# Performance work log

Hardware: AMD Instinct MI355X
Metric: run time of the kernel (lower is better)

## Reference

```python
import jax, jax.numpy as jnp
import numpy as np

DIM = 1024
N_HEADS = 16
HEAD_DIM = DIM // N_HEADS  # 64
B = 2
S = 2048
EPS = 1e-6  # flax LayerNorm default


def _layernorm(x, scale, bias):
    # LayerNorm over last axis with learnable scale and bias (flax defaults)
    mu = jnp.mean(x, axis=-1, keepdims=True)
    var = jnp.var(x, axis=-1, keepdims=True)
    return (x - mu) * jax.lax.rsqrt(var + EPS) * scale + bias


def _apply_rotary(t, sin, cos):
    # t: [b, s, h, hd]; sin/cos: [s, hd/2]
    tr = t.reshape(t.shape[:-1] + (-1, 2))
    r, i = tr[..., 0], tr[..., 1]            # [b, s, h, hd/2]
    c = cos[None, :, None, :]
    s_ = sin[None, :, None, :]
    out_r = r * c - i * s_
    out_i = r * s_ + i * c
    return jnp.stack([out_r, out_i], axis=-1).reshape(t.shape)


def setup_inputs() -> dict:
    key = jax.random.key(0)
    ks = jax.random.split(key, 8)
    x = jax.random.normal(ks[0], (B, S, DIM), dtype=jnp.float32)
    w_std = 1.0 / np.sqrt(DIM)  # ~lecun_normal scale
    wq = jax.random.normal(ks[1], (DIM, DIM), dtype=jnp.float32) * w_std
    wk = jax.random.normal(ks[2], (DIM, DIM), dtype=jnp.float32) * w_std
    wv = jax.random.normal(ks[3], (DIM, DIM), dtype=jnp.float32) * w_std
    wo = jax.random.normal(ks[4], (DIM, DIM), dtype=jnp.float32) * w_std
    # standard RoPE frequency table
    inv_freq = 1.0 / (10000.0 ** (np.arange(0, HEAD_DIM, 2, dtype=np.float32) / HEAD_DIM))  # [hd/2]
    angles = np.arange(S, dtype=np.float32)[:, None] * inv_freq[None, :]                    # [s, hd/2]
    return {
        "x": x,
        "freqs_sin": jnp.asarray(np.sin(angles), dtype=jnp.float32),
        "freqs_cos": jnp.asarray(np.cos(angles), dtype=jnp.float32),
        "wq": wq, "wk": wk, "wv": wv, "wo": wo,
        "q_scale": jnp.ones((DIM,), jnp.float32),
        "q_bias": jnp.zeros((DIM,), jnp.float32),
        "k_scale": jnp.ones((DIM,), jnp.float32),
        "k_bias": jnp.zeros((DIM,), jnp.float32),
    }


def reference(x, freqs_sin, freqs_cos, wq, wk, wv, wo, q_scale, q_bias, k_scale, k_bias):
    b, s, _ = x.shape
    xq = _layernorm(x @ wq, q_scale, q_bias).reshape(b, s, N_HEADS, HEAD_DIM)
    xk = _layernorm(x @ wk, k_scale, k_bias).reshape(b, s, N_HEADS, HEAD_DIM)
    xv = (x @ wv).reshape(b, s, N_HEADS, HEAD_DIM)
    xq = _apply_rotary(xq, freqs_sin, freqs_cos)
    xk = _apply_rotary(xk, freqs_sin, freqs_cos)
    scale = 1.0 / np.sqrt(HEAD_DIM)
    # non-causal SDPA, softmax in fp32 (force_fp32_for_softmax=True)
    logits = (jnp.einsum('bqhd,bkhd->bhqk', xq, xk) * scale).astype(jnp.float32)
    probs = jax.nn.softmax(logits, axis=-1).astype(xv.dtype)
    attn = jnp.einsum('bhqk,bkhd->bqhd', probs, xv).reshape(b, s, DIM)
    return attn @ wo
```

## Files before the change

### kernel.cpp

```cpp
#include <hip/hip_runtime.h>
#include <stddef.h>
#include <stdint.h>

#define DIM 1024
#define NH 16
#define HD 64
#define BATCH 2
#define SEQ 2048
#define ROWS (BATCH * SEQ)
#define KVB 64
#define NT (SEQ / KVB)

typedef short bf16x8 __attribute__((ext_vector_type(8)));
typedef float f32x4 __attribute__((ext_vector_type(4)));
typedef unsigned short u16;
typedef unsigned short u16x4v __attribute__((ext_vector_type(4)));

#define AS1 __attribute__((address_space(1)))
#define AS3 __attribute__((address_space(3)))

__device__ __forceinline__ void gload16(const u16* g, u16* l) {
  __builtin_amdgcn_global_load_lds((const AS1 void*)g, (AS3 void*)l, 16, 0, 0);
}

__device__ __forceinline__ u16 f2bf(float f) {
  union { float f; unsigned u; } v; v.f = f;
  unsigned r = v.u + 0x7FFFu + ((v.u >> 16) & 1u);
  return (u16)(r >> 16);
}

__global__ __launch_bounds__(256) void convert_x(const float* __restrict__ x,
                                                 u16* __restrict__ xb) {
  int i = (blockIdx.x * 256 + threadIdx.x) * 4;
  float4 v = *(const float4*)(x + i);
  u16x4v o;
  o.x = f2bf(v.x); o.y = f2bf(v.y); o.z = f2bf(v.z); o.w = f2bf(v.w);
  *(u16x4v*)(xb + i) = o;
}

__global__ __launch_bounds__(256) void transpose_w(
    const float* __restrict__ wq, const float* __restrict__ wk,
    const float* __restrict__ wv, const float* __restrict__ wo,
    u16* __restrict__ wqkvT, u16* __restrict__ woT) {
  __shared__ float tile[32][33];
  int bid = blockIdx.x;
  int mat = bid >> 10;
  int tIdx = bid & 1023;
  int tr = tIdx >> 5, tc = tIdx & 31;
  const float* src = mat == 0 ? wq : mat == 1 ? wk : mat == 2 ? wv : wo;
  int t = threadIdx.x;
#pragma unroll
  for (int i = 0; i < 4; ++i) {
    int idx = i * 256 + t;
    int r = idx >> 5, c = idx & 31;
    tile[r][c] = src[(tr * 32 + r) * DIM + tc * 32 + c];
  }
  __syncthreads();
  u16* dst = (mat < 3) ? (wqkvT + mat * DIM * DIM) : woT;
#pragma unroll
  for (int i = 0; i < 4; ++i) {
    int idx = i * 256 + t;
    int r = idx >> 5, c = idx & 31;
    dst[(tc * 32 + r) * DIM + tr * 32 + c] = f2bf(tile[c][r]);
  }
}

__global__ __launch_bounds__(256) void gemm_bt(
    const u16* __restrict__ A, const u16* __restrict__ BT,
    float* __restrict__ C, int M, int N, int K) {
  __shared__ u16 As[128 * 32];
  __shared__ u16 Bs[128 * 32];
  int ntn = N >> 7;
  int tm = blockIdx.x / ntn, tn = blockIdx.x % ntn;
  int m0 = tm << 7, n0 = tn << 7;
  int t = threadIdx.x;
  int w = t >> 6, lane = t & 63;
  int l15 = lane & 15, l4 = lane >> 4;
  int wr = w >> 1, wc = w & 1;

  f32x4 acc[4][4];
#pragma unroll
  for (int i = 0; i < 4; ++i)
#pragma unroll
    for (int j = 0; j < 4; ++j) acc[i][j] = (f32x4){0.f, 0.f, 0.f, 0.f};

  int srow = t >> 2, scol = (t & 3) << 3;
  const u16* Ag = A + (size_t)(m0 + srow) * K + scol;
  const u16* Bg = BT + (size_t)(n0 + srow) * K + scol;
  u16* Asl = &As[t * 8];
  u16* Bsl = &Bs[t * 8];
  size_t half = (size_t)64 * K;

  for (int kt = 0; kt < K; kt += 32) {
    __syncthreads();
    gload16(Ag + kt, Asl);
    gload16(Ag + half + kt, Asl + 2048);
    gload16(Bg + kt, Bsl);
    gload16(Bg + half + kt, Bsl + 2048);
    __syncthreads();
    bf16x8 af[4], bfr[4];
#pragma unroll
    for (int i = 0; i < 4; ++i)
      af[i] = *(const bf16x8*)(&As[(wr * 64 + i * 16 + l15) * 32 + l4 * 8]);
#pragma unroll
    for (int j = 0; j < 4; ++j)
      bfr[j] = *(const bf16x8*)(&Bs[(wc * 64 + j * 16 + l15) * 32 + l4 * 8]);
#pragma unroll
    for (int i = 0; i < 4; ++i)
#pragma unroll
      for (int j = 0; j < 4; ++j)
        acc[i][j] = __builtin_amdgcn_mfma_f32_16x16x32_bf16(af[i], bfr[j],
                                                            acc[i][j], 0, 0, 0);
  }
#pragma unroll
  for (int i = 0; i < 4; ++i)
#pragma unroll
    for (int j = 0; j < 4; ++j) {
      int m = m0 + wr * 64 + i * 16 + l4 * 4;
      int n = n0 + wc * 64 + j * 16 + l15;
#pragma unroll
      for (int r = 0; r < 4; ++r) C[(size_t)(m + r) * N + n] = acc[i][j][r];
    }
}

__global__ __launch_bounds__(256) void post_qk(
    const float* __restrict__ qkv, const float* __restrict__ fsin,
    const float* __restrict__ fcos, const float* __restrict__ qsc,
    const float* __restrict__ qbi, const float* __restrict__ ksc,
    const float* __restrict__ kbi, u16* __restrict__ Q, u16* __restrict__ Kk) {
  int row = blockIdx.x;
  int b = row >> 11, s = row & 2047;
  int t = threadIdx.x;
  const float* qrow = qkv + (size_t)row * 3072;
  const float* krow = qrow + DIM;
  float4 qv = *(const float4*)(qrow + t * 4);
  float4 kv = *(const float4*)(krow + t * 4);
  float qsum = qv.x + qv.y + qv.z + qv.w;
  float qss = qv.x * qv.x + qv.y * qv.y + qv.z * qv.z + qv.w * qv.w;
  float ksum = kv.x + kv.y + kv.z + kv.w;
  float kss = kv.x * kv.x + kv.y * kv.y + kv.z * kv.z + kv.w * kv.w;
#pragma unroll
  for (int off = 1; off < 64; off <<= 1) {
    qsum += __shfl_xor(qsum, off, 64);
    qss += __shfl_xor(qss, off, 64);
    ksum += __shfl_xor(ksum, off, 64);
    kss += __shfl_xor(kss, off, 64);
  }
  __shared__ float red[4][4];
  int w = t >> 6;
  if ((t & 63) == 0) {
    red[w][0] = qsum; red[w][1] = qss; red[w][2] = ksum; red[w][3] = kss;
  }
  __syncthreads();
  qsum = red[0][0] + red[1][0] + red[2][0] + red[3][0];
  qss = red[0][1] + red[1][1] + red[2][1] + red[3][1];
  ksum = red[0][2] + red[1][2] + red[2][2] + red[3][2];
  kss = red[0][3] + red[1][3] + red[2][3] + red[3][3];
  const float inv = 1.0f / 1024.0f;
  float muq = qsum * inv;
  float rq = rsqrtf(qss * inv - muq * muq + 1e-6f);
  float muk = ksum * inv;
  float rk = rsqrtf(kss * inv - muk * muk + 1e-6f);

  int e0 = t * 4;
  int h = e0 >> 6, d0 = e0 & 63;
  float q0 = (qv.x - muq) * rq * qsc[e0 + 0] + qbi[e0 + 0];
  float q1 = (qv.y - muq) * rq * qsc[e0 + 1] + qbi[e0 + 1];
  float q2 = (qv.z - muq) * rq * qsc[e0 + 2] + qbi[e0 + 2];
  float q3 = (qv.w - muq) * rq * qsc[e0 + 3] + qbi[e0 + 3];
  float k0 = (kv.x - muk) * rk * ksc[e0 + 0] + kbi[e0 + 0];
  float k1 = (kv.y - muk) * rk * ksc[e0 + 1] + kbi[e0 + 1];
  float k2 = (kv.z - muk) * rk * ksc[e0 + 2] + kbi[e0 + 2];
  float k3 = (kv.w - muk) * rk * ksc[e0 + 3] + kbi[e0 + 3];

  int p0 = d0 >> 1;
  float c0 = fcos[s * 32 + p0], s0 = fsin[s * 32 + p0];
  float c1 = fcos[s * 32 + p0 + 1], s1 = fsin[s * 32 + p0 + 1];
  float oq0 = q0 * c0 - q1 * s0, oq1 = q0 * s0 + q1 * c0;
  float oq2 = q2 * c1 - q3 * s1, oq3 = q2 * s1 + q3 * c1;
  float ok0 = k0 * c0 - k1 * s0, ok1 = k0 * s0 + k1 * c0;
  float ok2 = k2 * c1 - k3 * s1, ok3 = k2 * s1 + k3 * c1;

  const float QSC = 0.125f * 1.44269504088896340736f;
  u16x4v qo, ko;
  qo.x = f2bf(oq0 * QSC); qo.y = f2bf(oq1 * QSC);
  qo.z = f2bf(oq2 * QSC); qo.w = f2bf(oq3 * QSC);
  ko.x = f2bf(ok0); ko.y = f2bf(ok1); ko.z = f2bf(ok2); ko.w = f2bf(ok3);
  size_t base = ((size_t)(b * NH + h) * SEQ + s) * HD + d0;
  *(u16x4v*)(Q + base) = qo;
  *(u16x4v*)(Kk + base) = ko;
}

__global__ __launch_bounds__(256) void post_v(const float* __restrict__ qkv,
                                              u16* __restrict__ Vt) {
  __shared__ u16 vt[64][65];
  int bid = blockIdx.x;
  int st = bid & 31, bh = bid >> 5;
  int b = bh >> 4, h = bh & 15;
  int t = threadIdx.x;
#pragma unroll
  for (int i = 0; i < 16; ++i) {
    int idx = i * 256 + t;
    int ss = idx >> 6, d = idx & 63;
    float v = qkv[(size_t)(b * SEQ + st * 64 + ss) * 3072 + 2048 + h * 64 + d];
    vt[ss][d] = f2bf(v);
  }
  __syncthreads();
#pragma unroll
  for (int i = 0; i < 16; ++i) {
    int idx = i * 256 + t;
    int dd = idx >> 6, ss = idx & 63;
    Vt[((size_t)bh * 64 + dd) * SEQ + st * 64 + ss] = vt[ss][dd];
  }
}

__global__ __launch_bounds__(256) void attn_fwd(const u16* __restrict__ Q,
                                                const u16* __restrict__ K,
                                                const u16* __restrict__ Vt,
                                                u16* __restrict__ O) {
  __shared__ u16 Ks[2][64 * 64];
  __shared__ u16 Vs[2][64 * 64];
  __shared__ u16 P[4][16][80];

  int bid0 = blockIdx.x;
  int bid = (bid0 & 7) * 128 + (bid0 >> 3);
  int qb = bid & 31, bh = bid >> 5;
  int b = bh >> 4, h = bh & 15;
  int t = threadIdx.x;
  int w = t >> 6, lane = t & 63;
  int l15 = lane & 15, l4 = lane >> 4;
  int q0 = qb * 64 + w * 16;
  const u16* Qh = Q + (size_t)bh * SEQ * HD;
  const u16* Kh = K + (size_t)bh * SEQ * HD;
  const u16* Vh = Vt + (size_t)bh * HD * SEQ;

  int c0 = t, c1 = t + 256;
  int r0 = c0 >> 3, sc0 = ((c0 & 7) ^ (r0 & 7)) << 3;
  int r1 = c1 >> 3, sc1 = ((c1 & 7) ^ (r1 & 7)) << 3;
  const u16* Kg0 = Kh + (size_t)r0 * HD + sc0;
  const u16* Kg1 = Kh + (size_t)r1 * HD + sc1;
  const u16* Vg0 = Vh + (size_t)r0 * SEQ + sc0;
  const u16* Vg1 = Vh + (size_t)r1 * SEQ + sc1;

  gload16(Kg0, &Ks[0][c0 * 8]);
  gload16(Kg1, &Ks[0][c1 * 8]);
  gload16(Vg0, &Vs[0][c0 * 8]);
  gload16(Vg1, &Vs[0][c1 * 8]);

  bf16x8 qf[2];
#pragma unroll
  for (int kf = 0; kf < 2; ++kf)
    qf[kf] = *(const bf16x8*)(Qh + (size_t)(q0 + l15) * HD + kf * 32 + l4 * 8);

  f32x4 oacc[4];
#pragma unroll
  for (int df = 0; df < 4; ++df) oacc[df] = (f32x4){0.f, 0.f, 0.f, 0.f};
  float mrun = -1e30f, lpart = 0.f;

  __syncthreads();

  int buf = 0;
  for (int it = 0; it < NT; ++it) {
    if (it + 1 < NT) {
      size_t j0n = (size_t)(it + 1) * KVB;
      int nb = buf ^ 1;
      gload16(Kg0 + j0n * HD, &Ks[nb][c0 * 8]);
      gload16(Kg1 + j0n * HD, &Ks[nb][c1 * 8]);
      gload16(Vg0 + j0n, &Vs[nb][c0 * 8]);
      gload16(Vg1 + j0n, &Vs[nb][c1 * 8]);
    }
    const u16* Kb_ = Ks[buf];
    const u16* Vb_ = Vs[buf];
    f32x4 sacc[4];
#pragma unroll
    for (int nf = 0; nf < 4; ++nf) sacc[nf] = (f32x4){0.f, 0.f, 0.f, 0.f};
#pragma unroll
    for (int nf = 0; nf < 4; ++nf) {
      int row = nf * 16 + l15;
      int swz = (row & 7) << 3;
#pragma unroll
      for (int kf = 0; kf < 2; ++kf) {
        bf16x8 kfr =
            *(const bf16x8*)(&Kb_[row * 64 + ((kf * 32 + l4 * 8) ^ swz)]);
        sacc[nf] =
            __builtin_amdgcn_mfma_f32_16x16x32_bf16(kfr, qf[kf], sacc[nf], 0, 0, 0);
      }
    }
    bf16x8 vf[2][4];
#pragma unroll
    for (int df = 0; df < 4; ++df) {
      int row = df * 16 + l15;
      int swz = (row & 7) << 3;
#pragma unroll
      for (int kc = 0; kc < 2; ++kc)
        vf[kc][df] =
            *(const bf16x8*)(&Vb_[row * 64 + ((kc * 32 + l4 * 8) ^ swz)]);
    }
    float m16 = sacc[0][0];
#pragma unroll
    for (int nf = 0; nf < 4; ++nf)
#pragma unroll
      for (int r = 0; r < 4; ++r) m16 = fmaxf(m16, sacc[nf][r]);
    m16 = fmaxf(m16, __shfl_xor(m16, 16, 64));
    m16 = fmaxf(m16, __shfl_xor(m16, 32, 64));
    if (!__all(m16 - mrun <= 8.0f)) {
      float mnew = fmaxf(mrun, m16);
      float scl = exp2f(mrun - mnew);
      mrun = mnew;
      lpart *= scl;
      float sr[4];
#pragma unroll
      for (int r = 0; r < 4; ++r) sr[r] = __shfl(scl, l4 * 4 + r, 16);
#pragma unroll
      for (int df = 0; df < 4; ++df)
#pragma unroll
        for (int r = 0; r < 4; ++r) oacc[df][r] *= sr[r];
    }
    float rs = 0.f;
#pragma unroll
    for (int nf = 0; nf < 4; ++nf) {
      u16x4v pk;
#pragma unroll
      for (int r = 0; r < 4; ++r) {
        float pv = exp2f(sacc[nf][r] - mrun);
        rs += pv;
        pk[r] = f2bf(pv);
      }
      *(u16x4v*)(&P[w][l15][nf * 16 + l4 * 4]) = pk;
    }
    lpart += rs;
    asm volatile("s_waitcnt lgkmcnt(0)" ::: "memory");
    __builtin_amdgcn_sched_barrier(0);
#pragma unroll
    for (int kc = 0; kc < 2; ++kc) {
      bf16x8 pf = *(const bf16x8*)(&P[w][l15][kc * 32 + l4 * 8]);
#pragma unroll
      for (int df = 0; df < 4; ++df)
        oacc[df] =
            __builtin_amdgcn_mfma_f32_16x16x32_bf16(pf, vf[kc][df], oacc[df], 0, 0, 0);
    }
    __syncthreads();
    buf ^= 1;
  }
  lpart += __shfl_xor(lpart, 16, 64);
  lpart += __shfl_xor(lpart, 32, 64);
  float lr[4];
#pragma unroll
  for (int r = 0; r < 4; ++r) lr[r] = 1.0f / __shfl(lpart, l4 * 4 + r, 16);
#pragma unroll
  for (int df = 0; df < 4; ++df) {
    int dcol = h * 64 + df * 16 + l15;
#pragma unroll
    for (int r = 0; r < 4; ++r)
      O[(size_t)(b * SEQ + q0 + l4 * 4 + r) * DIM + dcol] = f2bf(oacc[df][r] * lr[r]);
  }
}

extern "C" void kernel_launch(void* const* d_in, const int* in_sizes, int n_in,
                              void* d_out, int out_size, void* d_ws,
                              size_t ws_size, hipStream_t stream) {
  const float* x = (const float*)d_in[0];
  const float* fsin = (const float*)d_in[1];
  const float* fcos = (const float*)d_in[2];
  const float* wq = (const float*)d_in[3];
  const float* wk = (const float*)d_in[4];
  const float* wv = (const float*)d_in[5];
  const float* wo = (const float*)d_in[6];
  const float* q_scale = (const float*)d_in[7];
  const float* q_bias = (const float*)d_in[8];
  const float* k_scale = (const float*)d_in[9];
  const float* k_bias = (const float*)d_in[10];
  float* out = (float*)d_out;

  u16* xb = (u16*)d_ws;
  u16* wqkvT = xb + (size_t)ROWS * DIM;
  u16* woT = wqkvT + (size_t)3 * DIM * DIM;
  float* qkv = (float*)(woT + (size_t)DIM * DIM);
  u16* Qb = (u16*)(qkv + (size_t)ROWS * 3 * DIM);
  u16* Kb = Qb + (size_t)BATCH * NH * SEQ * HD;
  u16* Vt = Kb + (size_t)BATCH * NH * SEQ * HD;
  u16* attnb = Vt + (size_t)BATCH * NH * SEQ * HD;

  convert_x<<<ROWS * DIM / 1024, 256, 0, stream>>>(x, xb);
  transpose_w<<<4 * 1024, 256, 0, stream>>>(wq, wk, wv, wo, wqkvT, woT);
  gemm_bt<<<(ROWS / 128) * (3 * DIM / 128), 256, 0, stream>>>(xb, wqkvT, qkv,
                                                              ROWS, 3 * DIM, DIM);
  post_qk<<<ROWS, 256, 0, stream>>>(qkv, fsin, fcos, q_scale, q_bias, k_scale,
                                    k_bias, Qb, Kb);
  post_v<<<BATCH * NH * (SEQ / 64), 256, 0, stream>>>(qkv, Vt);
  attn_fwd<<<BATCH * NH * (SEQ / 64), 256, 0, stream>>>(Qb, Kb, Vt, attnb);
  gemm_bt<<<(ROWS / 128) * (DIM / 128), 256, 0, stream>>>(attnb, woT, out, ROWS,
                                                          DIM, DIM);
}
```

Baseline: 274.9 us.

## Double attention KV tile to 128, split softmax/PV halves, fuse prep kernels

The attention kernel now stages 128 keys per iteration instead of 64, halving the number of loop iterations and barriers. Exponentiation and the PV MFMAs are split into two 64-key halves that reuse the per-wave P buffer, with s_setprio raising priority around the MFMA blocks. The x conversion and weight transpose kernels are merged into one launch, and the bf16 packing now uses the hip_bf16 intrinsics. The larger tiles double LDS use (about 64KB for K/V) and raise register pressure, which may lower occupancy.

```diff
diff --git a/kernel.cpp b/kernel.cpp
--- a/kernel.cpp
+++ b/kernel.cpp
@@ -1,4 +1,5 @@
 #include <hip/hip_runtime.h>
+#include <hip/hip_bf16.h>
 #include <stddef.h>
 #include <stdint.h>
 
@@ -8,7 +9,7 @@
 #define BATCH 2
 #define SEQ 2048
 #define ROWS (BATCH * SEQ)
-#define KVB 64
+#define KVB 128
 #define NT (SEQ / KVB)
 
 typedef short bf16x8 __attribute__((ext_vector_type(8)));
@@ -29,39 +30,40 @@
   return (u16)(r >> 16);
 }
 
-__global__ __launch_bounds__(256) void convert_x(const float* __restrict__ x,
-                                                 u16* __restrict__ xb) {
-  int i = (blockIdx.x * 256 + threadIdx.x) * 4;
-  float4 v = *(const float4*)(x + i);
-  u16x4v o;
-  o.x = f2bf(v.x); o.y = f2bf(v.y); o.z = f2bf(v.z); o.w = f2bf(v.w);
-  *(u16x4v*)(xb + i) = o;
-}
-
-__global__ __launch_bounds__(256) void transpose_w(
-    const float* __restrict__ wq, const float* __restrict__ wk,
-    const float* __restrict__ wv, const float* __restrict__ wo,
+__global__ __launch_bounds__(256) void prep(
+    const float* __restrict__ x, const float* __restrict__ wq,
+    const float* __restrict__ wk, const float* __restrict__ wv,
+    const float* __restrict__ wo, u16* __restrict__ xb,
     u16* __restrict__ wqkvT, u16* __restrict__ woT) {
   __shared__ float tile[32][33];
   int bid = blockIdx.x;
-  int mat = bid >> 10;
-  int tIdx = bid & 1023;
-  int tr = tIdx >> 5, tc = tIdx & 31;
-  const float* src = mat == 0 ? wq : mat == 1 ? wk : mat == 2 ? wv : wo;
   int t = threadIdx.x;
-#pragma unroll
-  for (int i = 0; i < 4; ++i) {
-    int idx = i * 256 + t;
-    int r = idx >> 5, c = idx & 31;
-    tile[r][c] = src[(tr * 32 + r) * DIM + tc * 32 + c];
-  }
-  __syncthreads();
-  u16* dst = (mat < 3) ? (wqkvT + mat * DIM * DIM) : woT;
-#pragma unroll
-  for (int i = 0; i < 4; ++i) {
-    int idx = i * 256 + t;
-    int r = idx >> 5, c = idx & 31;
-    dst[(tc * 32 + r) * DIM + tr * 32 + c] = f2bf(tile[c][r]);
+  if (bid < 4096) {
+    int i = (bid * 256 + t) * 4;
+    float4 v = *(const float4*)(x + i);
+    u16x4v o;
+    o.x = f2bf(v.x); o.y = f2bf(v.y); o.z = f2bf(v.z); o.w = f2bf(v.w);
+    *(u16x4v*)(xb + i) = o;
+  } else {
+    int bb = bid - 4096;
+    int mat = bb >> 10;
+    int tIdx = bb & 1023;
+    int tr = tIdx >> 5, tc = tIdx & 31;
+    const float* src = mat == 0 ? wq : mat == 1 ? wk : mat == 2 ? wv : wo;
+#pragma unroll
+    for (int i = 0; i < 4; ++i) {
+      int idx = i * 256 + t;
+      int r = idx >> 5, c = idx & 31;
+      tile[r][c] = src[(tr * 32 + r) * DIM + tc * 32 + c];
+    }
+    __syncthreads();
+    u16* dst = (mat < 3) ? (wqkvT + mat * DIM * DIM) : woT;
+#pragma unroll
+    for (int i = 0; i < 4; ++i) {
+      int idx = i * 256 + t;
+      int r = idx >> 5, c = idx & 31;
+      dst[(tc * 32 + r) * DIM + tr * 32 + c] = f2bf(tile[c][r]);
+    }
   }
 }
 
@@ -218,8 +220,8 @@
                                                 const u16* __restrict__ K,
                                                 const u16* __restrict__ Vt,
                                                 u16* __restrict__ O) {
-  __shared__ u16 Ks[2][64 * 64];
-  __shared__ u16 Vs[2][64 * 64];
+  __shared__ u16 Ks[2][KVB * HD];
+  __shared__ u16 Vs[2][HD * KVB];
   __shared__ u16 P[4][16][80];
 
   int bid0 = blockIdx.x;
@@ -234,18 +236,31 @@
   const u16* Kh = K + (size_t)bh * SEQ * HD;
   const u16* Vh = Vt + (size_t)bh * HD * SEQ;
 
-  int c0 = t, c1 = t + 256;
-  int r0 = c0 >> 3, sc0 = ((c0 & 7) ^ (r0 & 7)) << 3;
-  int r1 = c1 >> 3, sc1 = ((c1 & 7) ^ (r1 & 7)) << 3;
-  const u16* Kg0 = Kh + (size_t)r0 * HD + sc0;
-  const u16* Kg1 = Kh + (size_t)r1 * HD + sc1;
-  const u16* Vg0 = Vh + (size_t)r0 * SEQ + sc0;
-  const u16* Vg1 = Vh + (size_t)r1 * SEQ + sc1;
-
-  gload16(Kg0, &Ks[0][c0 * 8]);
-  gload16(Kg1, &Ks[0][c1 * 8]);
-  gload16(Vg0, &Vs[0][c0 * 8]);
-  gload16(Vg1, &Vs[0][c1 * 8]);
+  const u16* Kg[4];
+  const u16* Vg[4];
+#pragma unroll
+  for (int i = 0; i < 4; ++i) {
+    int c = t + 256 * i;
+    int kr = c >> 3, kcol = ((c & 7) ^ (kr & 7)) << 3;
+    Kg[i] = Kh + (size_t)kr * HD + kcol;
+    int vr = c >> 4, vcol = ((c & 15) ^ (vr & 7)) << 3;
+    Vg[i] = Vh + (size_t)vr * SEQ + vcol;
+  }
+
+#define STAGE(tile, bufi)                                  \
+  do {                                                     \
+    size_t j0s = (size_t)(tile) * KVB;                     \
+    gload16(Kg[0] + j0s * HD, &Ks[(bufi)][(t)*8]);         \
+    gload16(Kg[1] + j0s * HD, &Ks[(bufi)][(t + 256) * 8]); \
+    gload16(Kg[2] + j0s * HD, &Ks[(bufi)][(t + 512) * 8]); \
+    gload16(Kg[3] + j0s * HD, &Ks[(bufi)][(t + 768) * 8]); \
+    gload16(Vg[0] + j0s, &Vs[(bufi)][(t)*8]);              \
+    gload16(Vg[1] + j0s, &Vs[(bufi)][(t + 256) * 8]);      \
+    gload16(Vg[2] + j0s, &Vs[(bufi)][(t + 512) * 8]);      \
+    gload16(Vg[3] + j0s, &Vs[(bufi)][(t + 768) * 8]);      \
+  } while (0)
+
+  STAGE(0, 0);
 
   bf16x8 qf[2];
 #pragma unroll
@@ -261,21 +276,16 @@
 
   int buf = 0;
   for (int it = 0; it < NT; ++it) {
-    if (it + 1 < NT) {
-      size_t j0n = (size_t)(it + 1) * KVB;
-      int nb = buf ^ 1;
-      gload16(Kg0 + j0n * HD, &Ks[nb][c0 * 8]);
-      gload16(Kg1 + j0n * HD, &Ks[nb][c1 * 8]);
-      gload16(Vg0 + j0n, &Vs[nb][c0 * 8]);
-      gload16(Vg1 + j0n, &Vs[nb][c1 * 8]);
-    }
-    const u16* Kb_ = Ks[buf];
-    const u16* Vb_ = Vs[buf];
-    f32x4 sacc[4];
-#pragma unroll
-    for (int nf = 0; nf < 4; ++nf) sacc[nf] = (f32x4){0.f, 0.f, 0.f, 0.f};
-#pragma unroll
-    for (int nf = 0; nf < 4; ++nf) {
+    if (it + 1 < NT) STAGE(it + 1, buf ^ 1);
+    const u16* Kb_ = &Ks[buf][0];
+    const u16* Vb_ = &Vs[buf][0];
+
+    f32x4 sacc[8];
+#pragma unroll
+    for (int nf = 0; nf < 8; ++nf) sacc[nf] = (f32x4){0.f, 0.f, 0.f, 0.f};
+    __builtin_amdgcn_s_setprio(1);
+#pragma unroll
+    for (int nf = 0; nf < 8; ++nf) {
       int row = nf * 16 + l15;
       int swz = (row & 7) << 3;
 #pragma unroll
@@ -286,19 +296,22 @@
             __builtin_amdgcn_mfma_f32_16x16x32_bf16(kfr, qf[kf], sacc[nf], 0, 0, 0);
       }
     }
-    bf16x8 vf[2][4];
+    __builtin_amdgcn_s_setprio(0);
+
+    bf16x8 vf[4][4];
 #pragma unroll
     for (int df = 0; df < 4; ++df) {
       int row = df * 16 + l15;
       int swz = (row & 7) << 3;
 #pragma unroll
-      for (int kc = 0; kc < 2; ++kc)
+      for (int kc = 0; kc < 4; ++kc)
         vf[kc][df] =
-            *(const bf16x8*)(&Vb_[row * 64 + ((kc * 32 + l4 * 8) ^ swz)]);
-    }
+            *(const bf16x8*)(&Vb_[row * 128 + ((kc * 32 + l4 * 8) ^ swz)]);
+    }
+
     float m16 = sacc[0][0];
 #pragma unroll
-    for (int nf = 0; nf < 4; ++nf)
+    for (int nf = 0; nf < 8; ++nf)
 #pragma unroll
       for (int r = 0; r < 4; ++r) m16 = fmaxf(m16, sacc[nf][r]);
     m16 = fmaxf(m16, __shfl_xor(m16, 16, 64));
@@ -316,21 +329,26 @@
 #pragma unroll
         for (int r = 0; r < 4; ++r) oacc[df][r] *= sr[r];
     }
+
     float rs = 0.f;
 #pragma unroll
-    for (int nf = 0; nf < 4; ++nf) {
-      u16x4v pk;
-#pragma unroll
-      for (int r = 0; r < 4; ++r) {
-        float pv = exp2f(sacc[nf][r] - mrun);
-        rs += pv;
-        pk[r] = f2bf(pv);
-      }
-      *(u16x4v*)(&P[w][l15][nf * 16 + l4 * 4]) = pk;
-    }
-    lpart += rs;
+    for (int j = 0; j < 4; ++j) {
+      float p0 = exp2f(sacc[j][0] - mrun);
+      float p1 = exp2f(sacc[j][1] - mrun);
+      float p2 = exp2f(sacc[j][2] - mrun);
+      float p3 = exp2f(sacc[j][3] - mrun);
+      rs += (p0 + p1) + (p2 + p3);
+      __hip_bfloat162 pa, pb;
+      pa.x = __float2bfloat16(p0); pa.y = __float2bfloat16(p1);
+      pb.x = __float2bfloat16(p2); pb.y = __float2bfloat16(p3);
+      uint2 pk2;
+      pk2.x = *reinterpret_cast<unsigned int*>(&pa);
+      pk2.y = *reinterpret_cast<unsigned int*>(&pb);
+      *(uint2*)(&P[w][l15][j * 16 + l4 * 4]) = pk2;
+    }
     asm volatile("s_waitcnt lgkmcnt(0)" ::: "memory");
     __builtin_amdgcn_sched_barrier(0);
+    __builtin_amdgcn_s_setprio(1);
 #pragma unroll
     for (int kc = 0; kc < 2; ++kc) {
       bf16x8 pf = *(const bf16x8*)(&P[w][l15][kc * 32 + l4 * 8]);
@@ -339,9 +357,40 @@
         oacc[df] =
             __builtin_amdgcn_mfma_f32_16x16x32_bf16(pf, vf[kc][df], oacc[df], 0, 0, 0);
     }
+    __builtin_amdgcn_s_setprio(0);
+#pragma unroll
+    for (int j = 0; j < 4; ++j) {
+      float p0 = exp2f(sacc[4 + j][0] - mrun);
+      float p1 = exp2f(sacc[4 + j][1] - mrun);
+      float p2 = exp2f(sacc[4 + j][2] - mrun);
+      float p3 = exp2f(sacc[4 + j][3] - mrun);
+      rs += (p0 + p1) + (p2 + p3);
+      __hip_bfloat162 pa, pb;
+      pa.x = __float2bfloat16(p0); pa.y = __float2bfloat16(p1);
+      pb.x = __float2bfloat16(p2); pb.y = __float2bfloat16(p3);
+      uint2 pk2;
+      pk2.x = *reinterpret_cast<unsigned int*>(&pa);
+      pk2.y = *reinterpret_cast<unsigned int*>(&pb);
+      *(uint2*)(&P[w][l15][j * 16 + l4 * 4]) = pk2;
+    }
+    asm volatile("s_waitcnt lgkmcnt(0)" ::: "memory");
+    __builtin_amdgcn_sched_barrier(0);
+    __builtin_amdgcn_s_setprio(1);
+#pragma unroll
+    for (int kc = 0; kc < 2; ++kc) {
+      bf16x8 pf = *(const bf16x8*)(&P[w][l15][kc * 32 + l4 * 8]);
+#pragma unroll
+      for (int df = 0; df < 4; ++df)
+        oacc[df] = __builtin_amdgcn_mfma_f32_16x16x32_bf16(pf, vf[kc + 2][df],
+                                                           oacc[df], 0, 0, 0);
+    }
+    __builtin_amdgcn_s_setprio(0);
+
+    lpart += rs;
     __syncthreads();
     buf ^= 1;
   }
+#undef STAGE
   lpart += __shfl_xor(lpart, 16, 64);
   lpart += __shfl_xor(lpart, 32, 64);
   float lr[4];
@@ -381,8 +430,7 @@
   u16* Vt = Kb + (size_t)BATCH * NH * SEQ * HD;
   u16* attnb = Vt + (size_t)BATCH * NH * SEQ * HD;
 
-  convert_x<<<ROWS * DIM / 1024, 256, 0, stream>>>(x, xb);
-  transpose_w<<<4 * 1024, 256, 0, stream>>>(wq, wk, wv, wo, wqkvT, woT);
+  prep<<<8192, 256, 0, stream>>>(x, wq, wk, wv, wo, xb, wqkvT, woT);
   gemm_bt<<<(ROWS / 128) * (3 * DIM / 128), 256, 0, stream>>>(xb, wqkvT, qkv,
                                                               ROWS, 3 * DIM, DIM);
   post_qk<<<ROWS, 256, 0, stream>>>(qkv, fsin, fcos, q_scale, q_bias, k_scale,
```

New measurement: 267.1 us. -2.8%, faster.
